# Optimization experiments

Hardware: AMD Instinct MI355X
Metric: run time of the kernel (lower is better)

The kernel has to match this reference:

```python
import jax, jax.numpy as jnp
import numpy as np

T, B = 256, 64
VOCAB, EMBED, HIDDEN, LAYERS, TAGS = 50000, 512, 512, 2, 9
H = HIDDEN // 2  # per-direction hidden size


def setup_inputs() -> dict:
    key = jax.random.key(0)
    ks = jax.random.split(key, 11)
    s = 0.05
    embed_table = jax.random.normal(ks[1], (VOCAB, EMBED), dtype=jnp.float32) * s
    embed_table = embed_table.at[0].set(0.0)  # padding_idx=0 row is zero
    return {
        "x": jax.random.randint(ks[0], (T, B), 1, VOCAB),  # ids >=1 -> full lengths
        "embed_table": embed_table,
        "w_ih": jax.random.normal(ks[2], (LAYERS, 2, 4 * H, HIDDEN), dtype=jnp.float32) * s,
        "w_hh": jax.random.normal(ks[3], (LAYERS, 2, 4 * H, H), dtype=jnp.float32) * s,
        "b_ih": jax.random.normal(ks[4], (LAYERS, 2, 4 * H), dtype=jnp.float32) * s,
        "b_hh": jax.random.normal(ks[5], (LAYERS, 2, 4 * H), dtype=jnp.float32) * s,
        "out_w": jax.random.normal(ks[6], (TAGS, HIDDEN), dtype=jnp.float32) * s,
        "out_b": jax.random.normal(ks[7], (TAGS,), dtype=jnp.float32) * s,
        "start_trans": jax.random.normal(ks[8], (TAGS,), dtype=jnp.float32) * s,
        "end_trans": jax.random.normal(ks[9], (TAGS,), dtype=jnp.float32) * s,
        "trans": jax.random.normal(ks[10], (TAGS, TAGS), dtype=jnp.float32) * s,
    }


def _lstm_dir(xs, Wih, Whh, b, reverse):
    """One LSTM direction over time-major xs [T,B,D]; PyTorch gate order i,f,g,o."""
    bsz = xs.shape[1]
    h0 = jnp.zeros((bsz, H), xs.dtype)
    c0 = jnp.zeros((bsz, H), xs.dtype)

    def step(carry, xt):
        h, c = carry
        g = xt @ Wih.T + h @ Whh.T + b
        i, f, gg, o = jnp.split(g, 4, axis=-1)
        c = jax.nn.sigmoid(f) * c + jax.nn.sigmoid(i) * jnp.tanh(gg)
        h = jax.nn.sigmoid(o) * jnp.tanh(c)
        return (h, c), h

    _, hs = jax.lax.scan(step, (h0, c0), xs, reverse=reverse)
    return hs  # [T,B,H], aligned to input time order


def _emissions(x, embed_table, w_ih, w_hh, b_ih, b_hh, out_w, out_b):
    seq = embed_table[x]  # [T,B,EMBED]
    for l in range(LAYERS):
        fwd = _lstm_dir(seq, w_ih[l, 0], w_hh[l, 0], b_ih[l, 0] + b_hh[l, 0], False)
        bwd = _lstm_dir(seq, w_ih[l, 1], w_hh[l, 1], b_ih[l, 1] + b_hh[l, 1], True)
        seq = jnp.concatenate([fwd, bwd], axis=-1)  # [T,B,HIDDEN]
    return seq @ out_w.T + out_b  # [T,B,TAGS]


def reference(x, embed_table, w_ih, w_hh, b_ih, b_hh, out_w, out_b,
              start_trans, end_trans, trans):
    em = _emissions(x, embed_table, w_ih, w_hh, b_ih, b_hh, out_w, out_b)

    # Viterbi decode (all sequences full-length since ids >= 1)
    score0 = start_trans[None, :] + em[0]  # [B,TAGS]

    def vstep(score, em_t):
        tot = score[:, :, None] + trans[None, :, :]  # [B,prev,cur]
        best_prev = jnp.argmax(tot, axis=1)          # [B,cur]
        return jnp.max(tot, axis=1) + em_t, best_prev

    score, history = jax.lax.scan(vstep, score0, em[1:])  # history: [T-1,B,TAGS]
    score = score + end_trans[None, :]
    best_last = jnp.argmax(score, axis=-1)   # [B]
    best_score = jnp.max(score, axis=-1)     # [B]

    def btstep(tag, idx_t):
        prev = jnp.take_along_axis(idx_t, tag[:, None], axis=1)[:, 0]
        return prev, prev

    _, prevs = jax.lax.scan(btstep, best_last, history, reverse=True)  # [T-1,B]
    tags = jnp.concatenate([prevs, best_last[None, :]], axis=0)        # [T,B]
    return tags.T, best_score  # ([B,T] best paths, [B] path scores)
```

## Files before the change

### kernel.cpp

```cpp
#include <hip/hip_runtime.h>
#include <math.h>

#define TAGS 9

static __device__ __forceinline__ float sigmoidf_(float x) {
  return 1.0f / (1.0f + expf(-x));
}

__device__ __forceinline__ void st1_sc(float* p, float v) {
  asm volatile("global_store_dword %0, %1, off sc0 sc1" :: "v"(p), "v"(v) : "memory");
}
__device__ __forceinline__ void sti_sc(int* p, int v) {
  asm volatile("global_store_dword %0, %1, off sc0 sc1" :: "v"(p), "v"(v) : "memory");
}
__device__ __forceinline__ int ldi_sc(const int* p) {
  int r;
  asm volatile("global_load_dword %0, %1, off sc0 sc1" : "=v"(r) : "v"(p) : "memory");
  return r;
}
__device__ __forceinline__ void waitcnt0() {
  asm volatile("s_waitcnt vmcnt(0)" ::: "memory");
}

__global__ void k_pack_w(const float* __restrict__ whh, float* __restrict__ wPack) {
  int i = blockIdx.x * 256 + threadIdx.x;
  int rr = i & 15;
  int k = (i >> 4) & 255;
  int wg = (i >> 12) & 127;
  int L = i >> 19;
  int d = wg >> 6, ug = wg & 63;
  int row = d * 1024 + (rr >> 2) * 256 + ug * 4 + (rr & 3);
  wPack[i] = whh[(size_t)L * 524288 + (size_t)row * 256 + k];
}

__global__ void k_pack_ow(const float* __restrict__ out_w, float* __restrict__ owT) {
  int i = blockIdx.x * 256 + threadIdx.x;
  int tag = i % 9, ch = i / 9;
  owT[ch * 12 + tag] = out_w[tag * 512 + ch];
}

__global__ __launch_bounds__(256, 1)
void k_gatherT(const int* __restrict__ x, const float* __restrict__ table,
               float* __restrict__ seqT) {
  __shared__ float tile[64 * 513];
  __shared__ int x_s[64];
  int wg = blockIdx.x;
  int tid = threadIdx.x;
  int tb0 = wg * 64;
  if (tid < 64) x_s[tid] = x[tb0 + tid];
  __syncthreads();
#pragma unroll
  for (int i = 0; i < 32; i++) {
    int idx = tid + i * 256;
    int r = idx >> 7, c4 = (idx & 127) * 4;
    float4 v = *(const float4*)&table[(size_t)x_s[r] * 512 + c4];
    float* tp = &tile[r * 513 + c4];
    tp[0] = v.x; tp[1] = v.y; tp[2] = v.z; tp[3] = v.w;
  }
  __syncthreads();
#pragma unroll
  for (int i = 0; i < 128; i++) {
    int j = tid + i * 256;
    int ch = j >> 6, b = j & 63;
    seqT[(size_t)ch * 16384 + tb0 + b] = tile[b * 513 + ch];
  }
}

__global__ __launch_bounds__(256, 2)
void k_gemm_gates(const float* __restrict__ A, const float* __restrict__ seqT,
                  const float* __restrict__ bias1, const float* __restrict__ bias2,
                  float* __restrict__ gatesT) {
  __shared__ float As[16][132];
  __shared__ float Bs[16][132];
  int tid = threadIdx.x;
  int tx = tid & 15, ty = tid >> 4;
  int n0 = blockIdx.x * 128, m0 = blockIdx.y * 128;
  int lr = tid >> 2;
  int lk = (tid & 3) * 4;
  int bkk = tid >> 4, bn8 = (tid & 15) * 8;
  float acc[8][8];
#pragma unroll
  for (int i = 0; i < 8; i++)
#pragma unroll
    for (int j = 0; j < 8; j++) acc[i][j] = 0.f;
  const float* Ab = A + (size_t)m0 * 512;
  for (int k0 = 0; k0 < 512; k0 += 16) {
    float4 a0 = *(const float4*)&Ab[(size_t)lr * 512 + k0 + lk];
    float4 a1 = *(const float4*)&Ab[(size_t)(lr + 64) * 512 + k0 + lk];
    const float* Bp = seqT + (size_t)(k0 + bkk) * 16384 + n0 + bn8;
    float4 b0 = *(const float4*)Bp;
    float4 b1 = *(const float4*)(Bp + 4);
    __syncthreads();
    As[lk + 0][lr] = a0.x; As[lk + 1][lr] = a0.y; As[lk + 2][lr] = a0.z; As[lk + 3][lr] = a0.w;
    As[lk + 0][lr + 64] = a1.x; As[lk + 1][lr + 64] = a1.y; As[lk + 2][lr + 64] = a1.z; As[lk + 3][lr + 64] = a1.w;
    *(float4*)&Bs[bkk][bn8] = b0;
    *(float4*)&Bs[bkk][bn8 + 4] = b1;
    __syncthreads();
#pragma unroll
    for (int kk = 0; kk < 16; kk++) {
      float4 av0 = *(const float4*)&As[kk][ty * 4];
      float4 av1 = *(const float4*)&As[kk][ty * 4 + 64];
      float4 bv0 = *(const float4*)&Bs[kk][tx * 4];
      float4 bv1 = *(const float4*)&Bs[kk][tx * 4 + 64];
      float am[8] = {av0.x, av0.y, av0.z, av0.w, av1.x, av1.y, av1.z, av1.w};
      float bn[8] = {bv0.x, bv0.y, bv0.z, bv0.w, bv1.x, bv1.y, bv1.z, bv1.w};
#pragma unroll
      for (int i = 0; i < 8; i++)
#pragma unroll
        for (int j = 0; j < 8; j++) acc[i][j] += am[i] * bn[j];
    }
  }
  int t0 = n0 >> 6;
#pragma unroll
  for (int i = 0; i < 8; i++) {
    int m = m0 + ((i < 4) ? (ty * 4 + i) : (64 + ty * 4 + (i - 4)));
    float bs = bias1[m] + bias2[m];
    float4 o0 = {acc[i][0] + bs, acc[i][1] + bs, acc[i][2] + bs, acc[i][3] + bs};
    float4 o1 = {acc[i][4] + bs, acc[i][5] + bs, acc[i][6] + bs, acc[i][7] + bs};
    *(float4*)&gatesT[((size_t)t0 * 2048 + m) * 64 + tx * 4] = o0;
    *(float4*)&gatesT[((size_t)(t0 + 1) * 2048 + m) * 64 + tx * 4] = o1;
  }
}

__global__ __launch_bounds__(512, 1)
void k_lstm_rec(const float* __restrict__ gatesT,
                const float* __restrict__ wPack,
                float* __restrict__ seqT_out,
                float* __restrict__ hrot,
                int* __restrict__ flags,
                int layer) {
  __shared__ float p_s[8 * 16 * 64];
  int wg = blockIdx.x, tid = threadIdx.x;
  int d = wg >> 6;
  int u0 = (wg & 63) * 4;
  int b = tid & 63;
  int kq = __builtin_amdgcn_readfirstlane(tid >> 6);
  int uo = tid >> 6;
  const float4* wp4 = (const float4*)(wPack + ((size_t)wg * 256 + kq * 32) * 16);
  float c = 0.f;

  for (int tt = 0; tt < 256; ++tt) {
    int t = d ? 255 - tt : tt;
    float gin0 = 0.f, gin1 = 0.f, gin2 = 0.f, gin3 = 0.f;
    if (tid < 256) {
      const float* gp = gatesT + ((size_t)t * 2048 + d * 1024 + u0 + uo) * 64 + b;
      gin0 = gp[0 * 16384];
      gin1 = gp[1 * 16384];
      gin2 = gp[2 * 16384];
      gin3 = gp[3 * 16384];
    }
    const float* hcur = hrot + (size_t)tt * 32768 + (size_t)d * 16384 + kq * 2048 + b;
    float hreg[32];
#pragma unroll
    for (int j = 0; j < 32; j++) hreg[j] = hcur[j * 64];
    float acc[16];
#pragma unroll
    for (int r = 0; r < 16; r++) acc[r] = 0.f;
#pragma unroll 8
    for (int j = 0; j < 32; j++) {
      float hj = hreg[j];
      float4 w0 = wp4[j * 4 + 0];
      float4 w1 = wp4[j * 4 + 1];
      float4 w2 = wp4[j * 4 + 2];
      float4 w3 = wp4[j * 4 + 3];
      acc[0] += w0.x * hj;  acc[1] += w0.y * hj;  acc[2] += w0.z * hj;  acc[3] += w0.w * hj;
      acc[4] += w1.x * hj;  acc[5] += w1.y * hj;  acc[6] += w1.z * hj;  acc[7] += w1.w * hj;
      acc[8] += w2.x * hj;  acc[9] += w2.y * hj;  acc[10] += w2.z * hj; acc[11] += w2.w * hj;
      acc[12] += w3.x * hj; acc[13] += w3.y * hj; acc[14] += w3.z * hj; acc[15] += w3.w * hj;
    }
#pragma unroll
    for (int r = 0; r < 16; r++) p_s[(kq * 16 + r) * 64 + b] = acc[r];
    __syncthreads();
    if (tid < 256) {
      float gv[4] = {gin0, gin1, gin2, gin3};
#pragma unroll
      for (int g = 0; g < 4; g++) {
        int rr = g * 4 + uo;
        float s = gv[g];
#pragma unroll
        for (int q = 0; q < 8; q++) s += p_s[(q * 16 + rr) * 64 + b];
        gv[g] = s;
      }
      c = sigmoidf_(gv[1]) * c + sigmoidf_(gv[0]) * tanhf(gv[2]);
      float h = sigmoidf_(gv[3]) * tanhf(c);
      if (tt < 255) {
        float* hnext = hrot + (size_t)(tt + 1) * 32768 + (size_t)d * 16384;
        st1_sc(hnext + (u0 + uo) * 64 + b, h);
      }
      seqT_out[(size_t)(d * 256 + u0 + uo) * 16384 + t * 64 + b] = h;
    }
    if (tt < 255) {
      waitcnt0();
      __syncthreads();
      if (tid < 64) {
        int* fbase = flags + d * 16384 + tt * 64;
        int expect = layer * 256 + tt + 1;
        if (tid == 0) sti_sc(fbase + (wg & 63), expect);
        while (true) {
          int v = ldi_sc(fbase + tid);
          waitcnt0();
          if (__all(v == expect)) break;
          __builtin_amdgcn_s_sleep(1);
        }
      }
      __syncthreads();
    }
  }
}

__global__ __launch_bounds__(256, 4)
void k_emis(const float* __restrict__ seqT, const float* __restrict__ owT,
            const float* __restrict__ out_b, float* __restrict__ em) {
  int tb = blockIdx.x * 256 + threadIdx.x;
  float p[TAGS];
#pragma unroll
  for (int t = 0; t < TAGS; t++) p[t] = 0.f;
  for (int ch = 0; ch < 512; ch++) {
    float sv = seqT[(size_t)ch * 16384 + tb];
    const float4* o4 = (const float4*)(owT + ch * 12);
    float4 oa = o4[0], ob = o4[1];
    float oc = owT[ch * 12 + 8];
    p[0] += sv * oa.x; p[1] += sv * oa.y; p[2] += sv * oa.z; p[3] += sv * oa.w;
    p[4] += sv * ob.x; p[5] += sv * ob.y; p[6] += sv * ob.z; p[7] += sv * ob.w;
    p[8] += sv * oc;
  }
#pragma unroll
  for (int t = 0; t < TAGS; t++) em[(size_t)tb * TAGS + t] = p[t] + out_b[t];
}

__global__ void k_viterbi(const float* __restrict__ em, const float* __restrict__ start_t,
                          const float* __restrict__ end_t, const float* __restrict__ trans,
                          float* __restrict__ out) {
  int b = blockIdx.x;
  int lane = threadIdx.x;
  __shared__ unsigned char hist[255 * TAGS];
  float tin[TAGS];
#pragma unroll
  for (int p = 0; p < TAGS; p++) tin[p] = (lane < TAGS) ? trans[p * TAGS + lane] : 0.f;
  float score = -1e30f;
  if (lane < TAGS) score = start_t[lane] + em[(size_t)b * TAGS + lane];
  for (int t = 1; t < 256; t++) {
    float best = -1e30f; int bp = 0;
#pragma unroll
    for (int p = 0; p < TAGS; p++) {
      float v = __shfl(score, p, 64) + tin[p];
      if (v > best) { best = v; bp = p; }
    }
    if (lane < TAGS) {
      score = best + em[(size_t)(t * 64 + b) * TAGS + lane];
      hist[(t - 1) * TAGS + lane] = (unsigned char)bp;
    }
  }
  float fin = (lane < TAGS) ? (score + end_t[lane]) : -1e30f;
  float bsc = -1e30f; int bl = 0;
#pragma unroll
  for (int p = 0; p < TAGS; p++) {
    float v = __shfl(fin, p, 64);
    if (v > bsc) { bsc = v; bl = p; }
  }
  __syncthreads();
  if (lane == 0) {
    out[(size_t)16384 + b] = bsc;
    int tag = bl;
    out[(size_t)b * 256 + 255] = (float)tag;
    for (int t = 254; t >= 0; t--) {
      tag = hist[t * TAGS + tag];
      out[(size_t)b * 256 + t] = (float)tag;
    }
  }
}

extern "C" void kernel_launch(void* const* d_in, const int* in_sizes, int n_in,
                              void* d_out, int out_size, void* d_ws, size_t ws_size,
                              hipStream_t stream) {
  const int*   x       = (const int*)d_in[0];
  const float* table   = (const float*)d_in[1];
  const float* w_ih    = (const float*)d_in[2];
  const float* w_hh    = (const float*)d_in[3];
  const float* b_ih    = (const float*)d_in[4];
  const float* b_hh    = (const float*)d_in[5];
  const float* out_w   = (const float*)d_in[6];
  const float* out_b   = (const float*)d_in[7];
  const float* start_t = (const float*)d_in[8];
  const float* end_t   = (const float*)d_in[9];
  const float* trans   = (const float*)d_in[10];
  float* out = (float*)d_out;
  float* ws = (float*)d_ws;

  float* seqT0  = ws;
  float* seqT1  = seqT0 + 8388608;
  float* gatesT = seqT1 + 8388608;
  float* em     = gatesT;
  float* hrot   = gatesT + 33554432;
  float* wPack  = hrot + 8421376;
  float* owT    = wPack + 1048576;
  int*   flags  = (int*)(owT + 6144);

  hipMemsetAsync(hrot, 0, 32768 * sizeof(float), stream);

  k_pack_w<<<4096, 256, 0, stream>>>(w_hh, wPack);
  k_pack_ow<<<18, 256, 0, stream>>>(out_w, owT);
  k_gatherT<<<256, 256, 0, stream>>>(x, table, seqT0);

  dim3 gg(128, 16);
  k_gemm_gates<<<gg, 256, 0, stream>>>(w_ih, seqT0, b_ih, b_hh, gatesT);
  k_lstm_rec<<<128, 512, 0, stream>>>(gatesT, wPack, seqT1, hrot, flags, 0);
  k_gemm_gates<<<gg, 256, 0, stream>>>(w_ih + 1048576, seqT1, b_ih + 2048, b_hh + 2048, gatesT);
  k_lstm_rec<<<128, 512, 0, stream>>>(gatesT, wPack + 524288, seqT0, hrot, flags, 1);
  k_emis<<<64, 256, 0, stream>>>(seqT0, owT, out_b, em);
  k_viterbi<<<64, 64, 0, stream>>>(em, start_t, end_t, trans, out);
}
```

Before: 4.613 ms.

## Use sentinel-filled h buffer for data-driven sync and vectorized h loads

The h-state buffer is now pre-filled with a large sentinel value (0x7F bytes) before each layer. Consumers poll their own float4 slices until every value falls within a plausible range, which replaces waiting on stored data with a per-data validity check. The h layout becomes batch-major so each thread reads contiguous float4s, and the flags are padded to 16-int strides to avoid false sharing. The change also drops one waitcnt before the barrier. It relies on h values always satisfying |h|<1.5, which holds for the LSTM tanh output, and it adds two large memsets per call.

```diff
diff --git a/kernel.cpp b/kernel.cpp
--- a/kernel.cpp
+++ b/kernel.cpp
@@ -7,6 +7,11 @@
   return 1.0f / (1.0f + expf(-x));
 }
 
+__device__ __forceinline__ float4 ld4_sc(const float* p) {
+  float4 r;
+  asm volatile("global_load_dwordx4 %0, %1, off sc0 sc1" : "=v"(r) : "v"(p) : "memory");
+  return r;
+}
 __device__ __forceinline__ void st1_sc(float* p, float v) {
   asm volatile("global_store_dword %0, %1, off sc0 sc1" :: "v"(p), "v"(v) : "memory");
 }
@@ -20,6 +25,9 @@
 }
 __device__ __forceinline__ void waitcnt0() {
   asm volatile("s_waitcnt vmcnt(0)" ::: "memory");
+}
+__device__ __forceinline__ bool valid4(float4 v) {
+  return fabsf(v.x) < 1.5f && fabsf(v.y) < 1.5f && fabsf(v.z) < 1.5f && fabsf(v.w) < 1.5f;
 }
 
 __global__ void k_pack_w(const float* __restrict__ whh, float* __restrict__ wPack) {
@@ -149,24 +157,41 @@
       gin2 = gp[2 * 16384];
       gin3 = gp[3 * 16384];
     }
-    const float* hcur = hrot + (size_t)tt * 32768 + (size_t)d * 16384 + kq * 2048 + b;
-    float hreg[32];
-#pragma unroll
-    for (int j = 0; j < 32; j++) hreg[j] = hcur[j * 64];
+    const float* hp = hrot + (((size_t)tt * 2 + d) * 64 + b) * 256 + kq * 32;
+    const float4* hp4 = (const float4*)hp;
+    float4 hv[8];
+#pragma unroll
+    for (int j = 0; j < 8; j++) hv[j] = hp4[j];
+    unsigned bad = 0;
+#pragma unroll
+    for (int j = 0; j < 8; j++) bad |= valid4(hv[j]) ? 0u : (1u << j);
+    while (__any(bad)) {
+#pragma unroll
+      for (int j = 0; j < 8; j++) if (bad & (1u << j)) hv[j] = ld4_sc(hp + j * 4);
+      waitcnt0();
+#pragma unroll
+      for (int j = 0; j < 8; j++) if (valid4(hv[j])) bad &= ~(1u << j);
+      if (__any(bad)) __builtin_amdgcn_s_sleep(1);
+    }
     float acc[16];
 #pragma unroll
     for (int r = 0; r < 16; r++) acc[r] = 0.f;
-#pragma unroll 8
-    for (int j = 0; j < 32; j++) {
-      float hj = hreg[j];
-      float4 w0 = wp4[j * 4 + 0];
-      float4 w1 = wp4[j * 4 + 1];
-      float4 w2 = wp4[j * 4 + 2];
-      float4 w3 = wp4[j * 4 + 3];
-      acc[0] += w0.x * hj;  acc[1] += w0.y * hj;  acc[2] += w0.z * hj;  acc[3] += w0.w * hj;
-      acc[4] += w1.x * hj;  acc[5] += w1.y * hj;  acc[6] += w1.z * hj;  acc[7] += w1.w * hj;
-      acc[8] += w2.x * hj;  acc[9] += w2.y * hj;  acc[10] += w2.z * hj; acc[11] += w2.w * hj;
-      acc[12] += w3.x * hj; acc[13] += w3.y * hj; acc[14] += w3.z * hj; acc[15] += w3.w * hj;
+#pragma unroll 2
+    for (int jj = 0; jj < 8; jj++) {
+      float hq[4] = {hv[jj].x, hv[jj].y, hv[jj].z, hv[jj].w};
+#pragma unroll
+      for (int cc = 0; cc < 4; cc++) {
+        int j = jj * 4 + cc;
+        float hj = hq[cc];
+        float4 w0 = wp4[j * 4 + 0];
+        float4 w1 = wp4[j * 4 + 1];
+        float4 w2 = wp4[j * 4 + 2];
+        float4 w3 = wp4[j * 4 + 3];
+        acc[0] += w0.x * hj;  acc[1] += w0.y * hj;  acc[2] += w0.z * hj;  acc[3] += w0.w * hj;
+        acc[4] += w1.x * hj;  acc[5] += w1.y * hj;  acc[6] += w1.z * hj;  acc[7] += w1.w * hj;
+        acc[8] += w2.x * hj;  acc[9] += w2.y * hj;  acc[10] += w2.z * hj; acc[11] += w2.w * hj;
+        acc[12] += w3.x * hj; acc[13] += w3.y * hj; acc[14] += w3.z * hj; acc[15] += w3.w * hj;
+      }
     }
 #pragma unroll
     for (int r = 0; r < 16; r++) p_s[(kq * 16 + r) * 64 + b] = acc[r];
@@ -184,20 +209,18 @@
       c = sigmoidf_(gv[1]) * c + sigmoidf_(gv[0]) * tanhf(gv[2]);
       float h = sigmoidf_(gv[3]) * tanhf(c);
       if (tt < 255) {
-        float* hnext = hrot + (size_t)(tt + 1) * 32768 + (size_t)d * 16384;
-        st1_sc(hnext + (u0 + uo) * 64 + b, h);
+        st1_sc(hrot + (((size_t)(tt + 1) * 2 + d) * 64 + b) * 256 + u0 + uo, h);
       }
       seqT_out[(size_t)(d * 256 + u0 + uo) * 16384 + t * 64 + b] = h;
     }
     if (tt < 255) {
-      waitcnt0();
       __syncthreads();
+      int* fbase = flags + ((size_t)d * 256 + tt) * 1024;
+      int expect = layer * 256 + tt + 1;
+      if (tid == 0) sti_sc(fbase + (wg & 63) * 16, expect);
       if (tid < 64) {
-        int* fbase = flags + d * 16384 + tt * 64;
-        int expect = layer * 256 + tt + 1;
-        if (tid == 0) sti_sc(fbase + (wg & 63), expect);
         while (true) {
-          int v = ldi_sc(fbase + tid);
+          int v = ldi_sc(fbase + tid * 16);
           waitcnt0();
           if (__all(v == expect)) break;
           __builtin_amdgcn_s_sleep(1);
@@ -292,11 +315,12 @@
   float* gatesT = seqT1 + 8388608;
   float* em     = gatesT;
   float* hrot   = gatesT + 33554432;
-  float* wPack  = hrot + 8421376;
+  float* wPack  = hrot + 8388608;
   float* owT    = wPack + 1048576;
   int*   flags  = (int*)(owT + 6144);
 
-  hipMemsetAsync(hrot, 0, 32768 * sizeof(float), stream);
+  hipMemsetAsync(hrot, 0x7F, (size_t)8388608 * 4, stream);
+  hipMemsetAsync(hrot, 0, (size_t)32768 * 4, stream);
 
   k_pack_w<<<4096, 256, 0, stream>>>(w_hh, wPack);
   k_pack_ow<<<18, 256, 0, stream>>>(out_w, owT);
@@ -305,6 +329,7 @@
   dim3 gg(128, 16);
   k_gemm_gates<<<gg, 256, 0, stream>>>(w_ih, seqT0, b_ih, b_hh, gatesT);
   k_lstm_rec<<<128, 512, 0, stream>>>(gatesT, wPack, seqT1, hrot, flags, 0);
+  hipMemsetAsync(hrot + 32768, 0x7F, (size_t)(8388608 - 32768) * 4, stream);
   k_gemm_gates<<<gg, 256, 0, stream>>>(w_ih + 1048576, seqT1, b_ih + 2048, b_hh + 2048, gatesT);
   k_lstm_rec<<<128, 512, 0, stream>>>(gatesT, wPack + 524288, seqT0, hrot, flags, 1);
   k_emis<<<64, 256, 0, stream>>>(seqT0, owT, out_b, em);
```

Result: slower. 6.269 ms (+35.9%).
